# Optimization experiments

Measured on AMD Instinct MI355X. Metric: run time of the kernel, lower is better.

Reference implementation:

```python
import jax, jax.numpy as jnp
import numpy as np

DEPTH, HEADS, DIM_HEAD, DIM = 4, 8, 64, 512
B, N = 4, 512
SCALE = DIM_HEAD ** -0.5  # attention scale
EPS = 1e-5


def _ln(r, g, b):
    # naive real-valued LayerNorm over last dim
    m = jnp.mean(r, -1, keepdims=True)
    v = jnp.mean((r - m) ** 2, -1, keepdims=True)
    return (r - m) / jnp.sqrt(v + EPS) * g + b


def _cln(z, gr, br, gi, bi):
    # 'layer_norm_naive': LN applied separately to real and imag parts
    return jax.lax.complex(_ln(jnp.real(z), gr, br), _ln(jnp.imag(z), gi, bi))


def _csoftmax(z):
    # softmax on magnitude, phase preserved (Eq. 36, arXiv:1802.08026)
    p = jax.nn.softmax(jnp.abs(z), axis=-1)
    ph = jnp.angle(z)
    return jax.lax.complex(p * jnp.cos(ph), p * jnp.sin(ph))


def _crelu(z):
    return jax.lax.complex(jax.nn.relu(jnp.real(z)), jax.nn.relu(jnp.imag(z)))


def setup_inputs():
    key = jax.random.key(0)
    ks = jax.random.split(key, 8)
    s = np.float32(1.0 / np.sqrt(DIM))
    return dict(
        x_real=jax.random.normal(ks[0], (B, N, DIM), jnp.float32),
        x_imag=jax.random.normal(ks[1], (B, N, DIM), jnp.float32),
        ln1_g_r=jnp.ones((DEPTH, DIM), jnp.float32),
        ln1_b_r=jnp.zeros((DEPTH, DIM), jnp.float32),
        ln1_g_i=jnp.ones((DEPTH, DIM), jnp.float32),
        ln1_b_i=jnp.zeros((DEPTH, DIM), jnp.float32),
        ln2_g_r=jnp.ones((DEPTH, DIM), jnp.float32),
        ln2_b_r=jnp.zeros((DEPTH, DIM), jnp.float32),
        ln2_g_i=jnp.ones((DEPTH, DIM), jnp.float32),
        ln2_b_i=jnp.zeros((DEPTH, DIM), jnp.float32),
        qkv_w_r=jax.random.normal(ks[2], (DEPTH, DIM, DIM), jnp.float32) * s,
        qkv_w_i=jax.random.normal(ks[3], (DEPTH, DIM, DIM), jnp.float32) * s,
        out_w_r=jax.random.normal(ks[4], (DEPTH, DIM, DIM), jnp.float32) * s,
        out_w_i=jax.random.normal(ks[5], (DEPTH, DIM, DIM), jnp.float32) * s,
        out_b_r=jnp.zeros((DEPTH, DIM), jnp.float32),
        out_b_i=jnp.zeros((DEPTH, DIM), jnp.float32),
        ff_w_r=jax.random.normal(ks[6], (DEPTH, DIM, DIM), jnp.float32) * s,
        ff_w_i=jax.random.normal(ks[7], (DEPTH, DIM, DIM), jnp.float32) * s,
        step_size=jnp.full((DEPTH,), 0.1, jnp.float32),
        lambd=jnp.full((DEPTH,), 0.1, jnp.float32),
    )


def reference(x_real, x_imag,
              ln1_g_r, ln1_b_r, ln1_g_i, ln1_b_i,
              ln2_g_r, ln2_b_r, ln2_g_i, ln2_b_i,
              qkv_w_r, qkv_w_i, out_w_r, out_w_i, out_b_r, out_b_i,
              ff_w_r, ff_w_i, step_size, lambd):
    x = jax.lax.complex(x_real, x_imag)  # [B, N, DIM] complex64
    for l in range(DEPTH):
        Wqkv = jax.lax.complex(qkv_w_r[l], qkv_w_i[l])  # [inner, dim]
        Wout = jax.lax.complex(out_w_r[l], out_w_i[l])  # [dim, inner]
        bout = jax.lax.complex(out_b_r[l], out_b_i[l])
        Wff = jax.lax.complex(ff_w_r[l], ff_w_i[l])     # [dim, dim]
        # --- PreNorm + Attention (single shared QKV projection) + residual
        xn = _cln(x, ln1_g_r[l], ln1_b_r[l], ln1_g_i[l], ln1_b_i[l])
        w = jnp.einsum('bnd,ed->bne', xn, Wqkv)                 # complex linear, no bias
        w = w.reshape(B, N, HEADS, DIM_HEAD).transpose(0, 2, 1, 3)  # b h n d
        dots = jnp.einsum('bhnd,bhmd->bhnm', w, jnp.conj(w)) * SCALE
        attn = _csoftmax(dots)
        out = jnp.einsum('bhnm,bhmd->bhnd', attn, w)
        out = out.transpose(0, 2, 1, 3).reshape(B, N, HEADS * DIM_HEAD)
        out = jnp.einsum('bne,de->bnd', out, Wout) + bout
        x = out + x
        # --- PreNorm + ISTA-style FeedForward (CReLU); no outer residual
        xn = _cln(x, ln2_g_r[l], ln2_b_r[l], ln2_g_i[l], ln2_b_i[l])
        ss = jax.nn.softplus(step_size[l])
        lm = jax.nn.softplus(lambd[l])
        x1 = jnp.einsum('bnd,ed->bne', xn, Wff)
        x = _crelu(xn + ss * x1 - ss * lm)
    # stack real/imag so the output is a plain float tensor [2, B, N, DIM]
    return jnp.stack([jnp.real(x), jnp.imag(x)], axis=0)
```

## Files before the change

### kernel.cpp

```cpp
#include <hip/hip_runtime.h>
#include <math.h>

#define DEPTHL 4
#define HEADS 8
#define DH 64
#define DIM 512
#define BATCH 4
#define SEQ 512
#define ROWS (BATCH*SEQ)
#define SCALE 0.125f
#define LNEPS 1e-5f

typedef __attribute__((ext_vector_type(8))) short bfrag;
typedef __attribute__((ext_vector_type(4))) float ffrag;
#define MFMA(a,b,c) __builtin_amdgcn_mfma_f32_16x16x32_bf16(a, b, c, 0, 0, 0)

__device__ __forceinline__ unsigned short f2bf(float f) {
    unsigned int u = __float_as_uint(f);
    u += 0x7fffu + ((u >> 16) & 1u);
    return (unsigned short)(u >> 16);
}
__device__ __forceinline__ float bf2f(unsigned short b) {
    return __uint_as_float(((unsigned int)b) << 16);
}

__global__ __launch_bounds__(256) void convw(
    const float* __restrict__ s0, const float* __restrict__ s1,
    const float* __restrict__ s2, const float* __restrict__ s3,
    const float* __restrict__ s4, const float* __restrict__ s5,
    unsigned short* __restrict__ dst)
{
    int gid = blockIdx.x * 256 + threadIdx.x;
    int idx = gid * 4;
    int seg = idx >> 18;
    int off = idx & 262143;
    const float* s = seg == 0 ? s0 : seg == 1 ? s1 : seg == 2 ? s2 :
                     seg == 3 ? s3 : seg == 4 ? s4 : s5;
    float4 v = *(const float4*)(s + off);
    unsigned long long p = (unsigned long long)f2bf(v.x)
        | ((unsigned long long)f2bf(v.y) << 16)
        | ((unsigned long long)f2bf(v.z) << 32)
        | ((unsigned long long)f2bf(v.w) << 48);
    *(unsigned long long*)(dst + idx) = p;
}

__device__ __forceinline__ void blk_sum4(float& a, float& b, float& c, float& d) {
    __shared__ float s[16];
    #pragma unroll
    for (int o = 32; o; o >>= 1) {
        a += __shfl_xor(a, o); b += __shfl_xor(b, o);
        c += __shfl_xor(c, o); d += __shfl_xor(d, o);
    }
    int w = threadIdx.x >> 6;
    if ((threadIdx.x & 63) == 0) { s[w*4+0]=a; s[w*4+1]=b; s[w*4+2]=c; s[w*4+3]=d; }
    __syncthreads();
    a = s[0]+s[4]+s[8]+s[12];
    b = s[1]+s[5]+s[9]+s[13];
    c = s[2]+s[6]+s[10]+s[14];
    d = s[3]+s[7]+s[11]+s[15];
    __syncthreads();
}

__global__ __launch_bounds__(256) void ln_kernel(
    const float* __restrict__ xr, const float* __restrict__ xi,
    const float* __restrict__ gr, const float* __restrict__ br,
    const float* __restrict__ gi, const float* __restrict__ bi,
    unsigned short* __restrict__ outr, unsigned short* __restrict__ outi)
{
    int row = blockIdx.x, t = threadIdx.x;
    float2 vr = ((const float2*)(xr + (size_t)row*DIM))[t];
    float2 vi = ((const float2*)(xi + (size_t)row*DIM))[t];
    float sr = vr.x+vr.y, qr = vr.x*vr.x+vr.y*vr.y;
    float si = vi.x+vi.y, qi = vi.x*vi.x+vi.y*vi.y;
    blk_sum4(sr, qr, si, qi);
    float mr = sr*(1.f/DIM), mi_ = si*(1.f/DIM);
    float rr = 1.f/sqrtf(qr*(1.f/DIM)-mr*mr+LNEPS);
    float ri = 1.f/sqrtf(qi*(1.f/DIM)-mi_*mi_+LNEPS);
    float2 g2r = ((const float2*)gr)[t], b2r = ((const float2*)br)[t];
    float2 g2i = ((const float2*)gi)[t], b2i = ((const float2*)bi)[t];
    float o0 = (vr.x-mr)*rr*g2r.x + b2r.x;
    float o1 = (vr.y-mr)*rr*g2r.y + b2r.y;
    float o2 = (vi.x-mi_)*ri*g2i.x + b2i.x;
    float o3 = (vi.y-mi_)*ri*g2i.y + b2i.y;
    unsigned int pr = (unsigned int)f2bf(o0) | ((unsigned int)f2bf(o1) << 16);
    unsigned int pi = (unsigned int)f2bf(o2) | ((unsigned int)f2bf(o3) << 16);
    ((unsigned int*)(outr + (size_t)row*DIM))[t] = pr;
    ((unsigned int*)(outi + (size_t)row*DIM))[t] = pi;
}

template<int MODE>
__global__ __launch_bounds__(256) void cgemm_mfma(
    const unsigned short* __restrict__ Ar, const unsigned short* __restrict__ Ai,
    const unsigned short* __restrict__ Wr, const unsigned short* __restrict__ Wi,
    unsigned short* __restrict__ Obr, unsigned short* __restrict__ Obi,
    float* __restrict__ Ofr, float* __restrict__ Ofi,
    const float* __restrict__ biasR, const float* __restrict__ biasI,
    const float* __restrict__ stepp, const float* __restrict__ lamb, int layer)
{
    int tid = threadIdx.x;
    int lane = tid & 63;
    int w = tid >> 6, wr = w >> 1, wc = w & 1;
    int lrow = lane & 15, lg = lane >> 4;
    int bm = blockIdx.x, bn = blockIdx.y;

    const unsigned short* pA_r[2]; const unsigned short* pA_i[2];
    const unsigned short* pB_r[2]; const unsigned short* pB_i[2];
    #pragma unroll
    for (int t = 0; t < 2; ++t) {
        int arow = bm*64 + wr*32 + t*16 + lrow;
        int brow = bn*64 + wc*32 + t*16 + lrow;
        pA_r[t] = Ar + (size_t)arow*DIM + lg*8;
        pA_i[t] = Ai + (size_t)arow*DIM + lg*8;
        pB_r[t] = Wr + (size_t)brow*DIM + lg*8;
        pB_i[t] = Wi + (size_t)brow*DIM + lg*8;
    }
    ffrag acc1[2][2], acc2[2][2], acci[2][2];
    #pragma unroll
    for (int a = 0; a < 2; ++a)
    #pragma unroll
    for (int b = 0; b < 2; ++b) {
        acc1[a][b] = (ffrag){0.f,0.f,0.f,0.f};
        acc2[a][b] = (ffrag){0.f,0.f,0.f,0.f};
        acci[a][b] = (ffrag){0.f,0.f,0.f,0.f};
    }

    #pragma unroll 2
    for (int k0 = 0; k0 < DIM; k0 += 32) {
        bfrag a_r[2], a_i[2], b_r[2], b_i[2];
        #pragma unroll
        for (int t = 0; t < 2; ++t) {
            a_r[t] = *(const bfrag*)(pA_r[t] + k0);
            a_i[t] = *(const bfrag*)(pA_i[t] + k0);
            b_r[t] = *(const bfrag*)(pB_r[t] + k0);
            b_i[t] = *(const bfrag*)(pB_i[t] + k0);
        }
        #pragma unroll
        for (int mt = 0; mt < 2; ++mt)
        #pragma unroll
        for (int nt = 0; nt < 2; ++nt) {
            acc1[mt][nt] = MFMA(a_r[mt], b_r[nt], acc1[mt][nt]);
            acc2[mt][nt] = MFMA(a_i[mt], b_i[nt], acc2[mt][nt]);
            acci[mt][nt] = MFMA(a_r[mt], b_i[nt], acci[mt][nt]);
            acci[mt][nt] = MFMA(a_i[mt], b_r[nt], acci[mt][nt]);
        }
    }

    float ss = 0.f, sl = 0.f;
    if (MODE == 2) { ss = log1pf(expf(stepp[layer])); sl = ss * log1pf(expf(lamb[layer])); }

    #pragma unroll
    for (int mt = 0; mt < 2; ++mt)
    #pragma unroll
    for (int nt = 0; nt < 2; ++nt) {
        int E = bn*64 + wc*32 + nt*16 + lrow;
        #pragma unroll
        for (int r = 0; r < 4; ++r) {
            int R = bm*64 + wr*32 + mt*16 + lg*4 + r;
            float re = acc1[mt][nt][r] - acc2[mt][nt][r];
            float im = acci[mt][nt][r];
            if (MODE == 0) {
                int b = R >> 9, n = R & (SEQ-1);
                int h = E >> 6, d = E & 63;
                size_t off = (((size_t)(b*HEADS + h)*SEQ + n) << 6) + d;
                Obr[off] = f2bf(re);
                Obi[off] = f2bf(im);
            } else if (MODE == 1) {
                size_t off = (size_t)R*DIM + E;
                Ofr[off] = re + biasR[E] + Ofr[off];
                Ofi[off] = im + biasI[E] + Ofi[off];
            } else {
                size_t off = (size_t)R*DIM + E;
                float xnr_ = bf2f(Ar[off]), xni_ = bf2f(Ai[off]);
                Ofr[off] = fmaxf(xnr_ + ss*re - sl, 0.f);
                Ofi[off] = fmaxf(xni_ + ss*im, 0.f);
            }
        }
    }
}

__global__ __launch_bounds__(256) void attn_mfma(
    const unsigned short* __restrict__ whr, const unsigned short* __restrict__ whi,
    unsigned short* __restrict__ aor, unsigned short* __restrict__ aoi)
{
    __shared__ unsigned short sVr[64][40], sVi[64][40];
    __shared__ unsigned short sPr[4][16][40], sPi[4][16][40];
    __shared__ unsigned short sO[64][72];
    int tid = threadIdx.x, lane = tid & 63, w = tid >> 6;
    int lrow = lane & 15, lg = lane >> 4;
    int bh = blockIdx.x, qt = blockIdx.y;
    const unsigned short* baseR = whr + ((size_t)bh << 15);
    const unsigned short* baseI = whi + ((size_t)bh << 15);
    int q0 = qt*64 + w*16;

    bfrag qfr[2], qfi[2];
    #pragma unroll
    for (int ks = 0; ks < 2; ++ks) {
        qfr[ks] = *(const bfrag*)(baseR + ((size_t)(q0 + lrow) << 6) + ks*32 + lg*8);
        qfi[ks] = *(const bfrag*)(baseI + ((size_t)(q0 + lrow) << 6) + ks*32 + lg*8);
    }
    float M = -1e30f, S = 0.f;
    ffrag o1[4], o2[4], o3[4];
    #pragma unroll
    for (int dt = 0; dt < 4; ++dt) {
        o1[dt] = (ffrag){0.f,0.f,0.f,0.f};
        o2[dt] = (ffrag){0.f,0.f,0.f,0.f};
        o3[dt] = (ffrag){0.f,0.f,0.f,0.f};
    }
    int sm = tid & 31;
    int sd = (tid >> 5) * 8;

    #pragma unroll 1
    for (int m0 = 0; m0 < SEQ; m0 += 32) {
        __syncthreads();
        {
            bfrag vr = *(const bfrag*)(baseR + ((size_t)(m0 + sm) << 6) + sd);
            bfrag vi = *(const bfrag*)(baseI + ((size_t)(m0 + sm) << 6) + sd);
            #pragma unroll
            for (int j = 0; j < 8; ++j) {
                sVr[sd + j][sm] = (unsigned short)vr[j];
                sVi[sd + j][sm] = (unsigned short)vi[j];
            }
        }
        ffrag zr[2], zp[2], zm_[2];
        #pragma unroll
        for (int t = 0; t < 2; ++t) {
            zr[t] = (ffrag){0.f,0.f,0.f,0.f};
            zp[t] = (ffrag){0.f,0.f,0.f,0.f};
            zm_[t] = (ffrag){0.f,0.f,0.f,0.f};
        }
        #pragma unroll
        for (int t = 0; t < 2; ++t)
        #pragma unroll
        for (int ks = 0; ks < 2; ++ks) {
            bfrag kr = *(const bfrag*)(baseR + ((size_t)(m0 + t*16 + lrow) << 6) + ks*32 + lg*8);
            bfrag ki = *(const bfrag*)(baseI + ((size_t)(m0 + t*16 + lrow) << 6) + ks*32 + lg*8);
            zr[t]  = MFMA(kr, qfr[ks], zr[t]);
            zr[t]  = MFMA(ki, qfi[ks], zr[t]);
            zp[t]  = MFMA(kr, qfi[ks], zp[t]);
            zm_[t] = MFMA(ki, qfr[ks], zm_[t]);
        }
        float av[2][4], rv[2][4], iv[2][4];
        float pmax = -1e30f;
        #pragma unroll
        for (int t = 0; t < 2; ++t)
        #pragma unroll
        for (int r = 0; r < 4; ++r) {
            float zrv = zr[t][r] * SCALE;
            float ziv = (zp[t][r] - zm_[t][r]) * SCALE;
            float a = sqrtf(zrv*zrv + ziv*ziv);
            av[t][r] = a; rv[t][r] = zrv; iv[t][r] = ziv;
            pmax = fmaxf(pmax, a);
        }
        pmax = fmaxf(pmax, __shfl_xor(pmax, 16));
        pmax = fmaxf(pmax, __shfl_xor(pmax, 32));
        float Mnew = fmaxf(M, pmax);
        float f = expf(M - Mnew);
        M = Mnew;
        S *= f;
        #pragma unroll
        for (int dt = 0; dt < 4; ++dt) { o1[dt] *= f; o2[dt] *= f; o3[dt] *= f; }
        float ssum = 0.f;
        #pragma unroll
        for (int t = 0; t < 2; ++t) {
            float ur[4], ui[4];
            #pragma unroll
            for (int r = 0; r < 4; ++r) {
                float a = av[t][r];
                float ee = expf(a - M);
                ssum += ee;
                float inva = a > 0.f ? ee / a : 0.f;
                ur[r] = a > 0.f ? inva * rv[t][r] : ee;
                ui[r] = inva * iv[t][r];
            }
            uint2 wpr, wpi;
            wpr.x = (unsigned int)f2bf(ur[0]) | ((unsigned int)f2bf(ur[1]) << 16);
            wpr.y = (unsigned int)f2bf(ur[2]) | ((unsigned int)f2bf(ur[3]) << 16);
            wpi.x = (unsigned int)f2bf(ui[0]) | ((unsigned int)f2bf(ui[1]) << 16);
            wpi.y = (unsigned int)f2bf(ui[2]) | ((unsigned int)f2bf(ui[3]) << 16);
            *(uint2*)&sPr[w][lrow][t*16 + lg*4] = wpr;
            *(uint2*)&sPi[w][lrow][t*16 + lg*4] = wpi;
        }
        ssum += __shfl_xor(ssum, 16);
        ssum += __shfl_xor(ssum, 32);
        S += ssum;
        __syncthreads();
        bfrag pr = *(const bfrag*)&sPr[w][lrow][lg*8];
        bfrag pi = *(const bfrag*)&sPi[w][lrow][lg*8];
        #pragma unroll
        for (int dt = 0; dt < 4; ++dt) {
            bfrag vr = *(const bfrag*)&sVr[dt*16 + lrow][lg*8];
            bfrag vi = *(const bfrag*)&sVi[dt*16 + lrow][lg*8];
            o1[dt] = MFMA(vr, pr, o1[dt]);
            o2[dt] = MFMA(vi, pi, o2[dt]);
            o3[dt] = MFMA(vr, pi, o3[dt]);
            o3[dt] = MFMA(vi, pr, o3[dt]);
        }
    }

    float invS = 1.f / S;
    int b = bh >> 3, h = bh & 7;
    __syncthreads();
    #pragma unroll
    for (int dt = 0; dt < 4; ++dt) {
        uint2 p;
        p.x = (unsigned int)f2bf((o1[dt][0]-o2[dt][0])*invS)
            | ((unsigned int)f2bf((o1[dt][1]-o2[dt][1])*invS) << 16);
        p.y = (unsigned int)f2bf((o1[dt][2]-o2[dt][2])*invS)
            | ((unsigned int)f2bf((o1[dt][3]-o2[dt][3])*invS) << 16);
        *(uint2*)&sO[w*16 + lrow][dt*16 + lg*4] = p;
    }
    __syncthreads();
    {
        int qrow = tid >> 2, d0 = (tid & 3) * 16;
        bfrag v0 = *(const bfrag*)&sO[qrow][d0];
        bfrag v1 = *(const bfrag*)&sO[qrow][d0 + 8];
        size_t off = (((size_t)(b*SEQ + qt*64 + qrow)) << 9) + h*64 + d0;
        *(bfrag*)(aor + off) = v0;
        *(bfrag*)(aor + off + 8) = v1;
    }
    __syncthreads();
    #pragma unroll
    for (int dt = 0; dt < 4; ++dt) {
        uint2 p;
        p.x = (unsigned int)f2bf(o3[dt][0]*invS) | ((unsigned int)f2bf(o3[dt][1]*invS) << 16);
        p.y = (unsigned int)f2bf(o3[dt][2]*invS) | ((unsigned int)f2bf(o3[dt][3]*invS) << 16);
        *(uint2*)&sO[w*16 + lrow][dt*16 + lg*4] = p;
    }
    __syncthreads();
    {
        int qrow = tid >> 2, d0 = (tid & 3) * 16;
        bfrag v0 = *(const bfrag*)&sO[qrow][d0];
        bfrag v1 = *(const bfrag*)&sO[qrow][d0 + 8];
        size_t off = (((size_t)(b*SEQ + qt*64 + qrow)) << 9) + h*64 + d0;
        *(bfrag*)(aoi + off) = v0;
        *(bfrag*)(aoi + off + 8) = v1;
    }
}

extern "C" void kernel_launch(void* const* d_in, const int* in_sizes, int n_in,
                              void* d_out, int out_size, void* d_ws, size_t ws_size,
                              hipStream_t stream)
{
    const float* x_real  = (const float*)d_in[0];
    const float* x_imag  = (const float*)d_in[1];
    const float* ln1_g_r = (const float*)d_in[2];
    const float* ln1_b_r = (const float*)d_in[3];
    const float* ln1_g_i = (const float*)d_in[4];
    const float* ln1_b_i = (const float*)d_in[5];
    const float* ln2_g_r = (const float*)d_in[6];
    const float* ln2_b_r = (const float*)d_in[7];
    const float* ln2_g_i = (const float*)d_in[8];
    const float* ln2_b_i = (const float*)d_in[9];
    const float* qkv_w_r = (const float*)d_in[10];
    const float* qkv_w_i = (const float*)d_in[11];
    const float* out_w_r = (const float*)d_in[12];
    const float* out_w_i = (const float*)d_in[13];
    const float* out_b_r = (const float*)d_in[14];
    const float* out_b_i = (const float*)d_in[15];
    const float* ff_w_r  = (const float*)d_in[16];
    const float* ff_w_i  = (const float*)d_in[17];
    const float* stepp   = (const float*)d_in[18];
    const float* lamb    = (const float*)d_in[19];

    const size_t SZ = (size_t)ROWS * DIM;
    const size_t WSEG = (size_t)DIM * DIM;
    float* xr = (float*)d_ws;
    float* xi = xr + SZ;
    unsigned short* xnr = (unsigned short*)(xi + SZ);
    unsigned short* xni = xnr + SZ;
    unsigned short* whr = xni + SZ;
    unsigned short* whi = whr + SZ;
    unsigned short* aor = whi + SZ;
    unsigned short* aoi = aor + SZ;
    unsigned short* wb  = aoi + SZ;

    hipMemcpyAsync(xr, x_real, SZ*sizeof(float), hipMemcpyDeviceToDevice, stream);
    hipMemcpyAsync(xi, x_imag, SZ*sizeof(float), hipMemcpyDeviceToDevice, stream);

    for (int l = 0; l < DEPTHL; ++l) {
        const size_t WO = (size_t)l * WSEG;
        convw<<<1536, 256, 0, stream>>>(qkv_w_r + WO, qkv_w_i + WO, out_w_r + WO,
                                        out_w_i + WO, ff_w_r + WO, ff_w_i + WO, wb);
        ln_kernel<<<ROWS, 256, 0, stream>>>(xr, xi,
            ln1_g_r + l*DIM, ln1_b_r + l*DIM, ln1_g_i + l*DIM, ln1_b_i + l*DIM, xnr, xni);
        cgemm_mfma<0><<<dim3(32, 8), 256, 0, stream>>>(xnr, xni, wb, wb + WSEG,
            whr, whi, nullptr, nullptr, nullptr, nullptr, nullptr, nullptr, l);
        attn_mfma<<<dim3(32, 8), 256, 0, stream>>>(whr, whi, aor, aoi);
        cgemm_mfma<1><<<dim3(32, 8), 256, 0, stream>>>(aor, aoi, wb + 2*WSEG, wb + 3*WSEG,
            nullptr, nullptr, xr, xi, out_b_r + l*DIM, out_b_i + l*DIM, nullptr, nullptr, l);
        ln_kernel<<<ROWS, 256, 0, stream>>>(xr, xi,
            ln2_g_r + l*DIM, ln2_b_r + l*DIM, ln2_g_i + l*DIM, ln2_b_i + l*DIM, xnr, xni);
        cgemm_mfma<2><<<dim3(32, 8), 256, 0, stream>>>(xnr, xni, wb + 4*WSEG, wb + 5*WSEG,
            nullptr, nullptr, xr, xi, nullptr, nullptr, stepp, lamb, l);
    }
    hipMemcpyAsync(d_out, xr, SZ*sizeof(float), hipMemcpyDeviceToDevice, stream);
    hipMemcpyAsync((float*)d_out + SZ, xi, SZ*sizeof(float), hipMemcpyDeviceToDevice, stream);
}
```

Before: 610.0 us.

## Hoist weight conversion, retile GEMMs, pre-transpose V, single-wave attention blocks

```diff
diff --git a/kernel.cpp b/kernel.cpp
--- a/kernel.cpp
+++ b/kernel.cpp
@@ -13,6 +13,8 @@
 
 typedef __attribute__((ext_vector_type(8))) short bfrag;
 typedef __attribute__((ext_vector_type(4))) float ffrag;
+typedef __attribute__((ext_vector_type(4))) unsigned short u16x4;
+typedef __attribute__((ext_vector_type(8))) unsigned short u16x8;
 #define MFMA(a,b,c) __builtin_amdgcn_mfma_f32_16x16x32_bf16(a, b, c, 0, 0, 0)
 
 __device__ __forceinline__ unsigned short f2bf(float f) {
@@ -30,10 +32,9 @@
     const float* __restrict__ s4, const float* __restrict__ s5,
     unsigned short* __restrict__ dst)
 {
-    int gid = blockIdx.x * 256 + threadIdx.x;
-    int idx = gid * 4;
-    int seg = idx >> 18;
-    int off = idx & 262143;
+    size_t idx = ((size_t)blockIdx.x * 256 + threadIdx.x) * 4;
+    int seg = (int)(idx >> 20);
+    int off = (int)(idx & 1048575);
     const float* s = seg == 0 ? s0 : seg == 1 ? s1 : seg == 2 ? s2 :
                      seg == 3 ? s3 : seg == 4 ? s4 : s5;
     float4 v = *(const float4*)(s + off);
@@ -89,7 +90,7 @@
 }
 
 template<int MODE>
-__global__ __launch_bounds__(256) void cgemm_mfma(
+__global__ __launch_bounds__(512, 4) void cgemm_mfma(
     const unsigned short* __restrict__ Ar, const unsigned short* __restrict__ Ai,
     const unsigned short* __restrict__ Wr, const unsigned short* __restrict__ Wi,
     unsigned short* __restrict__ Obr, unsigned short* __restrict__ Obi,
@@ -99,98 +100,112 @@
 {
     int tid = threadIdx.x;
     int lane = tid & 63;
-    int w = tid >> 6, wr = w >> 1, wc = w & 1;
+    int w = tid >> 6, wr = w >> 2, wc = w & 3;
     int lrow = lane & 15, lg = lane >> 4;
     int bm = blockIdx.x, bn = blockIdx.y;
 
-    const unsigned short* pA_r[2]; const unsigned short* pA_i[2];
-    const unsigned short* pB_r[2]; const unsigned short* pB_i[2];
-    #pragma unroll
-    for (int t = 0; t < 2; ++t) {
-        int arow = bm*64 + wr*32 + t*16 + lrow;
-        int brow = bn*64 + wc*32 + t*16 + lrow;
-        pA_r[t] = Ar + (size_t)arow*DIM + lg*8;
-        pA_i[t] = Ai + (size_t)arow*DIM + lg*8;
-        pB_r[t] = Wr + (size_t)brow*DIM + lg*8;
-        pB_i[t] = Wi + (size_t)brow*DIM + lg*8;
-    }
-    ffrag acc1[2][2], acc2[2][2], acci[2][2];
-    #pragma unroll
-    for (int a = 0; a < 2; ++a)
-    #pragma unroll
-    for (int b = 0; b < 2; ++b) {
-        acc1[a][b] = (ffrag){0.f,0.f,0.f,0.f};
-        acc2[a][b] = (ffrag){0.f,0.f,0.f,0.f};
-        acci[a][b] = (ffrag){0.f,0.f,0.f,0.f};
-    }
-
-    #pragma unroll 2
-    for (int k0 = 0; k0 < DIM; k0 += 32) {
-        bfrag a_r[2], a_i[2], b_r[2], b_i[2];
-        #pragma unroll
-        for (int t = 0; t < 2; ++t) {
-            a_r[t] = *(const bfrag*)(pA_r[t] + k0);
-            a_i[t] = *(const bfrag*)(pA_i[t] + k0);
-            b_r[t] = *(const bfrag*)(pB_r[t] + k0);
-            b_i[t] = *(const bfrag*)(pB_i[t] + k0);
-        }
-        #pragma unroll
-        for (int mt = 0; mt < 2; ++mt)
-        #pragma unroll
-        for (int nt = 0; nt < 2; ++nt) {
-            acc1[mt][nt] = MFMA(a_r[mt], b_r[nt], acc1[mt][nt]);
-            acc2[mt][nt] = MFMA(a_i[mt], b_i[nt], acc2[mt][nt]);
-            acci[mt][nt] = MFMA(a_r[mt], b_i[nt], acci[mt][nt]);
-            acci[mt][nt] = MFMA(a_i[mt], b_r[nt], acci[mt][nt]);
-        }
-    }
+    const unsigned short* pAr = Ar + (size_t)(bm*32 + wr*16 + lrow)*DIM + lg*8;
+    const unsigned short* pAi = Ai + (size_t)(bm*32 + wr*16 + lrow)*DIM + lg*8;
+    const unsigned short* pBr = Wr + (size_t)(bn*64 + wc*16 + lrow)*DIM + lg*8;
+    const unsigned short* pBi = Wi + (size_t)(bn*64 + wc*16 + lrow)*DIM + lg*8;
+
+    ffrag acc1 = (ffrag){0.f,0.f,0.f,0.f};
+    ffrag acc2 = (ffrag){0.f,0.f,0.f,0.f};
+    ffrag acci = (ffrag){0.f,0.f,0.f,0.f};
+
+    bfrag a_r = *(const bfrag*)(pAr);
+    bfrag a_i = *(const bfrag*)(pAi);
+    bfrag b_r = *(const bfrag*)(pBr);
+    bfrag b_i = *(const bfrag*)(pBi);
+
+    #pragma unroll 4
+    for (int k0 = 0; k0 < DIM - 32; k0 += 32) {
+        bfrag na_r = *(const bfrag*)(pAr + k0 + 32);
+        bfrag na_i = *(const bfrag*)(pAi + k0 + 32);
+        bfrag nb_r = *(const bfrag*)(pBr + k0 + 32);
+        bfrag nb_i = *(const bfrag*)(pBi + k0 + 32);
+        acc1 = MFMA(a_r, b_r, acc1);
+        acc2 = MFMA(a_i, b_i, acc2);
+        acci = MFMA(a_r, b_i, acci);
+        acci = MFMA(a_i, b_r, acci);
+        a_r = na_r; a_i = na_i; b_r = nb_r; b_i = nb_i;
+    }
+    acc1 = MFMA(a_r, b_r, acc1);
+    acc2 = MFMA(a_i, b_i, acc2);
+    acci = MFMA(a_r, b_i, acci);
+    acci = MFMA(a_i, b_r, acci);
 
     float ss = 0.f, sl = 0.f;
     if (MODE == 2) { ss = log1pf(expf(stepp[layer])); sl = ss * log1pf(expf(lamb[layer])); }
 
-    #pragma unroll
-    for (int mt = 0; mt < 2; ++mt)
-    #pragma unroll
-    for (int nt = 0; nt < 2; ++nt) {
-        int E = bn*64 + wc*32 + nt*16 + lrow;
-        #pragma unroll
-        for (int r = 0; r < 4; ++r) {
-            int R = bm*64 + wr*32 + mt*16 + lg*4 + r;
-            float re = acc1[mt][nt][r] - acc2[mt][nt][r];
-            float im = acci[mt][nt][r];
-            if (MODE == 0) {
-                int b = R >> 9, n = R & (SEQ-1);
-                int h = E >> 6, d = E & 63;
-                size_t off = (((size_t)(b*HEADS + h)*SEQ + n) << 6) + d;
-                Obr[off] = f2bf(re);
-                Obi[off] = f2bf(im);
-            } else if (MODE == 1) {
-                size_t off = (size_t)R*DIM + E;
-                Ofr[off] = re + biasR[E] + Ofr[off];
-                Ofi[off] = im + biasI[E] + Ofi[off];
-            } else {
-                size_t off = (size_t)R*DIM + E;
-                float xnr_ = bf2f(Ar[off]), xni_ = bf2f(Ai[off]);
-                Ofr[off] = fmaxf(xnr_ + ss*re - sl, 0.f);
-                Ofi[off] = fmaxf(xni_ + ss*im, 0.f);
-            }
-        }
-    }
-}
-
-__global__ __launch_bounds__(256) void attn_mfma(
+    int E = bn*64 + wc*16 + lrow;
+    #pragma unroll
+    for (int r = 0; r < 4; ++r) {
+        int R = bm*32 + wr*16 + lg*4 + r;
+        float re = acc1[r] - acc2[r];
+        float im = acci[r];
+        if (MODE == 0) {
+            int b = R >> 9, n = R & (SEQ-1);
+            int h = E >> 6, d = E & 63;
+            size_t off = (((size_t)(b*HEADS + h)*SEQ + n) << 6) + d;
+            Obr[off] = f2bf(re);
+            Obi[off] = f2bf(im);
+        } else if (MODE == 1) {
+            size_t off = (size_t)R*DIM + E;
+            Ofr[off] = re + biasR[E] + Ofr[off];
+            Ofi[off] = im + biasI[E] + Ofi[off];
+        } else {
+            size_t off = (size_t)R*DIM + E;
+            float xnr_ = bf2f(Ar[off]), xni_ = bf2f(Ai[off]);
+            Ofr[off] = fmaxf(xnr_ + ss*re - sl, 0.f);
+            Ofi[off] = fmaxf(xni_ + ss*im, 0.f);
+        }
+    }
+}
+
+__global__ __launch_bounds__(256) void vT_kernel(
     const unsigned short* __restrict__ whr, const unsigned short* __restrict__ whi,
+    unsigned short* __restrict__ whTr, unsigned short* __restrict__ whTi)
+{
+    __shared__ unsigned short sR[64][68], sI[64][68];
+    int tid = threadIdx.x, mt = blockIdx.x, bh = blockIdx.y;
+    const unsigned short* bR = whr + ((size_t)bh << 15) + (size_t)(mt << 6) * 64;
+    const unsigned short* bI = whi + ((size_t)bh << 15) + (size_t)(mt << 6) * 64;
+    int ml = tid >> 4, d4 = (tid & 15) * 4;
+    #pragma unroll
+    for (int jj = 0; jj < 4; ++jj) {
+        int r_ = ml + jj*16;
+        *(u16x4*)&sR[r_][d4] = *(const u16x4*)(bR + r_*64 + d4);
+        *(u16x4*)&sI[r_][d4] = *(const u16x4*)(bI + r_*64 + d4);
+    }
+    __syncthreads();
+    int d = tid >> 2, mo = (tid & 3) * 16;
+    u16x8 vr0, vr1, vi0, vi1;
+    #pragma unroll
+    for (int jj = 0; jj < 8; ++jj) {
+        vr0[jj] = sR[mo + jj][d];      vr1[jj] = sR[mo + 8 + jj][d];
+        vi0[jj] = sI[mo + jj][d];      vi1[jj] = sI[mo + 8 + jj][d];
+    }
+    size_t off = ((size_t)bh*64 + d)*512 + (mt << 6) + mo;
+    *(u16x8*)(whTr + off) = vr0;  *(u16x8*)(whTr + off + 8) = vr1;
+    *(u16x8*)(whTi + off) = vi0;  *(u16x8*)(whTi + off + 8) = vi1;
+}
+
+__global__ __launch_bounds__(64) void attn_mfma(
+    const unsigned short* __restrict__ whr, const unsigned short* __restrict__ whi,
+    const unsigned short* __restrict__ whTr, const unsigned short* __restrict__ whTi,
     unsigned short* __restrict__ aor, unsigned short* __restrict__ aoi)
 {
-    __shared__ unsigned short sVr[64][40], sVi[64][40];
-    __shared__ unsigned short sPr[4][16][40], sPi[4][16][40];
-    __shared__ unsigned short sO[64][72];
-    int tid = threadIdx.x, lane = tid & 63, w = tid >> 6;
+    __shared__ __align__(16) unsigned short sP[2][16][40];
+    __shared__ __align__(16) unsigned short sO[16][68];
+    int lane = threadIdx.x;
     int lrow = lane & 15, lg = lane >> 4;
     int bh = blockIdx.x, qt = blockIdx.y;
     const unsigned short* baseR = whr + ((size_t)bh << 15);
     const unsigned short* baseI = whi + ((size_t)bh << 15);
-    int q0 = qt*64 + w*16;
+    const unsigned short* vTr = whTr + ((size_t)bh << 15);
+    const unsigned short* vTi = whTi + ((size_t)bh << 15);
+    int q0 = qt*16;
 
     bfrag qfr[2], qfi[2];
     #pragma unroll
@@ -206,20 +221,14 @@
         o2[dt] = (ffrag){0.f,0.f,0.f,0.f};
         o3[dt] = (ffrag){0.f,0.f,0.f,0.f};
     }
-    int sm = tid & 31;
-    int sd = (tid >> 5) * 8;
 
     #pragma unroll 1
     for (int m0 = 0; m0 < SEQ; m0 += 32) {
-        __syncthreads();
-        {
-            bfrag vr = *(const bfrag*)(baseR + ((size_t)(m0 + sm) << 6) + sd);
-            bfrag vi = *(const bfrag*)(baseI + ((size_t)(m0 + sm) << 6) + sd);
-            #pragma unroll
-            for (int j = 0; j < 8; ++j) {
-                sVr[sd + j][sm] = (unsigned short)vr[j];
-                sVi[sd + j][sm] = (unsigned short)vi[j];
-            }
+        bfrag vfr[4], vfi[4];
+        #pragma unroll
+        for (int dt = 0; dt < 4; ++dt) {
+            vfr[dt] = *(const bfrag*)(vTr + (size_t)(dt*16 + lrow)*512 + m0 + lg*8);
+            vfi[dt] = *(const bfrag*)(vTi + (size_t)(dt*16 + lrow)*512 + m0 + lg*8);
         }
         ffrag zr[2], zp[2], zm_[2];
         #pragma unroll
@@ -277,29 +286,25 @@
             wpr.y = (unsigned int)f2bf(ur[2]) | ((unsigned int)f2bf(ur[3]) << 16);
             wpi.x = (unsigned int)f2bf(ui[0]) | ((unsigned int)f2bf(ui[1]) << 16);
             wpi.y = (unsigned int)f2bf(ui[2]) | ((unsigned int)f2bf(ui[3]) << 16);
-            *(uint2*)&sPr[w][lrow][t*16 + lg*4] = wpr;
-            *(uint2*)&sPi[w][lrow][t*16 + lg*4] = wpi;
+            *(uint2*)&sP[0][lrow][t*16 + lg*4] = wpr;
+            *(uint2*)&sP[1][lrow][t*16 + lg*4] = wpi;
         }
         ssum += __shfl_xor(ssum, 16);
         ssum += __shfl_xor(ssum, 32);
         S += ssum;
-        __syncthreads();
-        bfrag pr = *(const bfrag*)&sPr[w][lrow][lg*8];
-        bfrag pi = *(const bfrag*)&sPi[w][lrow][lg*8];
+        bfrag pr = *(const bfrag*)&sP[0][lrow][lg*8];
+        bfrag pi = *(const bfrag*)&sP[1][lrow][lg*8];
         #pragma unroll
         for (int dt = 0; dt < 4; ++dt) {
-            bfrag vr = *(const bfrag*)&sVr[dt*16 + lrow][lg*8];
-            bfrag vi = *(const bfrag*)&sVi[dt*16 + lrow][lg*8];
-            o1[dt] = MFMA(vr, pr, o1[dt]);
-            o2[dt] = MFMA(vi, pi, o2[dt]);
-            o3[dt] = MFMA(vr, pi, o3[dt]);
-            o3[dt] = MFMA(vi, pr, o3[dt]);
+            o1[dt] = MFMA(vfr[dt], pr, o1[dt]);
+            o2[dt] = MFMA(vfi[dt], pi, o2[dt]);
+            o3[dt] = MFMA(vfr[dt], pi, o3[dt]);
+            o3[dt] = MFMA(vfi[dt], pr, o3[dt]);
         }
     }
 
     float invS = 1.f / S;
     int b = bh >> 3, h = bh & 7;
-    __syncthreads();
     #pragma unroll
     for (int dt = 0; dt < 4; ++dt) {
         uint2 p;
@@ -307,33 +312,30 @@
             | ((unsigned int)f2bf((o1[dt][1]-o2[dt][1])*invS) << 16);
         p.y = (unsigned int)f2bf((o1[dt][2]-o2[dt][2])*invS)
             | ((unsigned int)f2bf((o1[dt][3]-o2[dt][3])*invS) << 16);
-        *(uint2*)&sO[w*16 + lrow][dt*16 + lg*4] = p;
-    }
-    __syncthreads();
+        *(uint2*)&sO[lrow][dt*16 + lg*4] = p;
+    }
     {
-        int qrow = tid >> 2, d0 = (tid & 3) * 16;
-        bfrag v0 = *(const bfrag*)&sO[qrow][d0];
-        bfrag v1 = *(const bfrag*)&sO[qrow][d0 + 8];
-        size_t off = (((size_t)(b*SEQ + qt*64 + qrow)) << 9) + h*64 + d0;
-        *(bfrag*)(aor + off) = v0;
-        *(bfrag*)(aor + off + 8) = v1;
-    }
-    __syncthreads();
+        int q = lane >> 2, d0 = (lane & 3) * 16;
+        u16x8 v0 = *(const u16x8*)&sO[q][d0];
+        u16x8 v1 = *(const u16x8*)&sO[q][d0 + 8];
+        size_t off = (((size_t)(b*SEQ + q0 + q)) << 9) + h*64 + d0;
+        *(u16x8*)(aor + off) = v0;
+        *(u16x8*)(aor + off + 8) = v1;
+    }
     #pragma unroll
     for (int dt = 0; dt < 4; ++dt) {
         uint2 p;
         p.x = (unsigned int)f2bf(o3[dt][0]*invS) | ((unsigned int)f2bf(o3[dt][1]*invS) << 16);
         p.y = (unsigned int)f2bf(o3[dt][2]*invS) | ((unsigned int)f2bf(o3[dt][3]*invS) << 16);
-        *(uint2*)&sO[w*16 + lrow][dt*16 + lg*4] = p;
-    }
-    __syncthreads();
+        *(uint2*)&sO[lrow][dt*16 + lg*4] = p;
+    }
     {
-        int qrow = tid >> 2, d0 = (tid & 3) * 16;
-        bfrag v0 = *(const bfrag*)&sO[qrow][d0];
-        bfrag v1 = *(const bfrag*)&sO[qrow][d0 + 8];
-        size_t off = (((size_t)(b*SEQ + qt*64 + qrow)) << 9) + h*64 + d0;
-        *(bfrag*)(aoi + off) = v0;
-        *(bfrag*)(aoi + off + 8) = v1;
+        int q = lane >> 2, d0 = (lane & 3) * 16;
+        u16x8 v0 = *(const u16x8*)&sO[q][d0];
+        u16x8 v1 = *(const u16x8*)&sO[q][d0 + 8];
+        size_t off = (((size_t)(b*SEQ + q0 + q)) << 9) + h*64 + d0;
+        *(u16x8*)(aoi + off) = v0;
+        *(u16x8*)(aoi + off + 8) = v1;
     }
 }
 
@@ -364,35 +366,49 @@
 
     const size_t SZ = (size_t)ROWS * DIM;
     const size_t WSEG = (size_t)DIM * DIM;
+    const size_t WALL = 4 * WSEG;
     float* xr = (float*)d_ws;
     float* xi = xr + SZ;
-    unsigned short* xnr = (unsigned short*)(xi + SZ);
-    unsigned short* xni = xnr + SZ;
-    unsigned short* whr = xni + SZ;
-    unsigned short* whi = whr + SZ;
-    unsigned short* aor = whi + SZ;
-    unsigned short* aoi = aor + SZ;
-    unsigned short* wb  = aoi + SZ;
+    unsigned short* xnr  = (unsigned short*)(xi + SZ);
+    unsigned short* xni  = xnr + SZ;
+    unsigned short* whr  = xni + SZ;
+    unsigned short* whi  = whr + SZ;
+    unsigned short* aor  = whi + SZ;
+    unsigned short* aoi  = aor + SZ;
+    unsigned short* whTr = aoi + SZ;
+    unsigned short* whTi = whTr + SZ;
+    unsigned short* wb   = whTi + SZ;
+
+    float* outR = (float*)d_out;
+    float* outI = outR + SZ;
 
     hipMemcpyAsync(xr, x_real, SZ*sizeof(float), hipMemcpyDeviceToDevice, stream);
     hipMemcpyAsync(xi, x_imag, SZ*sizeof(float), hipMemcpyDeviceToDevice, stream);
 
+    convw<<<6144, 256, 0, stream>>>(qkv_w_r, qkv_w_i, out_w_r, out_w_i, ff_w_r, ff_w_i, wb);
+
     for (int l = 0; l < DEPTHL; ++l) {
         const size_t WO = (size_t)l * WSEG;
-        convw<<<1536, 256, 0, stream>>>(qkv_w_r + WO, qkv_w_i + WO, out_w_r + WO,
-                                        out_w_i + WO, ff_w_r + WO, ff_w_i + WO, wb);
+        const unsigned short* Wq_r = wb + 0*WALL + WO;
+        const unsigned short* Wq_i = wb + 1*WALL + WO;
+        const unsigned short* Wo_r = wb + 2*WALL + WO;
+        const unsigned short* Wo_i = wb + 3*WALL + WO;
+        const unsigned short* Wf_r = wb + 4*WALL + WO;
+        const unsigned short* Wf_i = wb + 5*WALL + WO;
+
         ln_kernel<<<ROWS, 256, 0, stream>>>(xr, xi,
             ln1_g_r + l*DIM, ln1_b_r + l*DIM, ln1_g_i + l*DIM, ln1_b_i + l*DIM, xnr, xni);
-        cgemm_mfma<0><<<dim3(32, 8), 256, 0, stream>>>(xnr, xni, wb, wb + WSEG,
+        cgemm_mfma<0><<<dim3(64, 8), 512, 0, stream>>>(xnr, xni, Wq_r, Wq_i,
             whr, whi, nullptr, nullptr, nullptr, nullptr, nullptr, nullptr, l);
-        attn_mfma<<<dim3(32, 8), 256, 0, stream>>>(whr, whi, aor, aoi);
-        cgemm_mfma<1><<<dim3(32, 8), 256, 0, stream>>>(aor, aoi, wb + 2*WSEG, wb + 3*WSEG,
+        vT_kernel<<<dim3(8, 32), 256, 0, stream>>>(whr, whi, whTr, whTi);
+        attn_mfma<<<dim3(32, 32), 64, 0, stream>>>(whr, whi, whTr, whTi, aor, aoi);
+        cgemm_mfma<1><<<dim3(64, 8), 512, 0, stream>>>(aor, aoi, Wo_r, Wo_i,
             nullptr, nullptr, xr, xi, out_b_r + l*DIM, out_b_i + l*DIM, nullptr, nullptr, l);
         ln_kernel<<<ROWS, 256, 0, stream>>>(xr, xi,
             ln2_g_r + l*DIM, ln2_b_r + l*DIM, ln2_g_i + l*DIM, ln2_b_i + l*DIM, xnr, xni);
-        cgemm_mfma<2><<<dim3(32, 8), 256, 0, stream>>>(xnr, xni, wb + 4*WSEG, wb + 5*WSEG,
-            nullptr, nullptr, xr, xi, nullptr, nullptr, stepp, lamb, l);
-    }
-    hipMemcpyAsync(d_out, xr, SZ*sizeof(float), hipMemcpyDeviceToDevice, stream);
-    hipMemcpyAsync((float*)d_out + SZ, xi, SZ*sizeof(float), hipMemcpyDeviceToDevice, stream);
-}
+        float* dstR = (l == DEPTHL-1) ? outR : xr;
+        float* dstI = (l == DEPTHL-1) ? outI : xi;
+        cgemm_mfma<2><<<dim3(64, 8), 512, 0, stream>>>(xnr, xni, Wf_r, Wf_i,
+            nullptr, nullptr, dstR, dstI, nullptr, nullptr, stepp, lamb, l);
+    }
+}
```

Result: slower. 689.9 us (+13.1%).
